# Kernel tuning notes

Measured on AMD Instinct MI355X. Metric: run time of the kernel, lower is better.

## Reference

```python
import jax, jax.numpy as jnp
import numpy as np

B, S, D = 4, 2048, 1024


def setup_inputs() -> dict:
    key = jax.random.key(0)
    kq, k1, k2, k3 = jax.random.split(key, 4)
    w_scale = 1.0 / np.sqrt(D)  # ~ glorot scale for square Dense
    q = jax.random.normal(kq, (B, S, D), dtype=jnp.float32)
    Wq = jax.random.normal(k1, (D, D), dtype=jnp.float32) * w_scale
    Wk = jax.random.normal(k2, (D, D), dtype=jnp.float32) * w_scale  # unused in self-attn path (bug in original)
    Wv = jax.random.normal(k3, (D, D), dtype=jnp.float32) * w_scale
    # causal mask: 1 = masked (future), matching tf.where(mask == 1, -1e9, scores)
    mask = jnp.triu(jnp.ones((S, S), dtype=jnp.int32), k=1)
    return {"q": q, "Wq": Wq, "Wk": Wk, "Wv": Wv, "mask": mask}


def reference(q, Wq, Wk, Wv, mask):
    # Self-attention path of the original: k=None, v=None.
    WQ = jnp.einsum('bsd,de->bse', q, Wq)
    # Faithful to the original code: dense_v is applied for BOTH K and V.
    WKV = jnp.einsum('bsd,de->bse', q, Wv)
    d_k = jnp.asarray(D, dtype=q.dtype)
    scores = jnp.einsum('bqd,bkd->bqk', WQ, WKV) / jnp.sqrt(d_k)  # [B,S,S]
    scores = jnp.where(mask == 1, jnp.asarray(-1e9, scores.dtype), scores)
    attn = jax.nn.softmax(scores, axis=-1)
    return jnp.einsum('bqk,bkd->bqd', attn, WKV)
```

## Files before the change

kernel.cpp:

```cpp
#include <hip/hip_runtime.h>


typedef unsigned short u16;
typedef short short8 __attribute__((ext_vector_type(8)));
typedef float floatx4 __attribute__((ext_vector_type(4)));

#define S_LEN 2048
#define D_DIM 1024
#define BK 64

__device__ inline u16 f2b(float f) {
  unsigned u = __float_as_uint(f);
  return (u16)((u + 0x7fffu + ((u >> 16) & 1u)) >> 16);
}

__device__ __forceinline__ void gload16(const u16* g, u16* l) {
  __builtin_amdgcn_global_load_lds(
      (const __attribute__((address_space(1))) void*)g,
      (__attribute__((address_space(3))) void*)l, 16, 0, 0);
}

__global__ __launch_bounds__(256)
void prep(const float* __restrict__ q, u16* __restrict__ qb16,
          const float* __restrict__ Wq, u16* __restrict__ Wqt,
          const float* __restrict__ Wv, u16* __restrict__ Wvt,
          float* __restrict__ rowsum) {
  int id = blockIdx.x, tid = threadIdx.x;
  if (id < 4096) {
    if (id < 4) {
      int o = id * 2048 + tid * 8;
      float4 zz = {0.f, 0.f, 0.f, 0.f};
      *(float4*)&rowsum[o] = zz;
      *(float4*)&rowsum[o + 4] = zz;
    }
    size_t idx = ((size_t)id * 256 + tid) * 8;
    float4 a0 = *(const float4*)&q[idx];
    float4 a1 = *(const float4*)&q[idx + 4];
    short8 v;
    v[0] = (short)f2b(a0.x); v[1] = (short)f2b(a0.y);
    v[2] = (short)f2b(a0.z); v[3] = (short)f2b(a0.w);
    v[4] = (short)f2b(a1.x); v[5] = (short)f2b(a1.y);
    v[6] = (short)f2b(a1.z); v[7] = (short)f2b(a1.w);
    *(short8*)&qb16[idx] = v;
    return;
  }
  __shared__ u16 tile[64][65];
  int id2 = id - 4096;
  int z = id2 >> 8;
  int idx4 = id2 & 255;
  int c0 = (idx4 & 15) * 64, r0 = (idx4 >> 4) * 64;
  const float* src = z ? Wv : Wq;
  u16* dst = z ? Wvt : Wqt;
  int tx = tid & 63, ty = tid >> 6;
#pragma unroll
  for (int i = 0; i < 16; ++i)
    tile[i * 4 + ty][tx] =
        f2b(src[(size_t)(r0 + i * 4 + ty) * 1024 + (c0 + tx)]);
  __syncthreads();
#pragma unroll
  for (int i = 0; i < 16; ++i)
    dst[(size_t)(c0 + i * 4 + ty) * 1024 + (r0 + tx)] = tile[tx][i * 4 + ty];
}

__global__ __launch_bounds__(512, 2)
void gemm_proj(const u16* __restrict__ A, const u16* __restrict__ B0,
               const u16* __restrict__ B1, u16* __restrict__ C0,
               u16* __restrict__ C1, u16* __restrict__ WKVt) {
  __shared__ __align__(16) u16 lds[65536];

  int id = blockIdx.x;
  int xcd = id & 7, i5 = id >> 3;
  int m_idx = xcd * 4 + (i5 & 3);
  int n_idx = i5 >> 2;
  int z = n_idx >> 2;
  int n0 = (n_idx & 3) * 256;
  int m0 = m_idx * 256;
  const u16* Bp = z ? B1 : B0;
  u16* Cp = z ? C1 : C0;

  int tid = threadIdx.x;
  int wv = tid >> 6, lane = tid & 63, quad = lane >> 4, l15 = lane & 15;
  int wm = wv >> 2, wn = wv & 3;

  int off_g[2];
#pragma unroll
  for (int l = 0; l < 2; ++l) {
    int chunk = (wv * 2 + l) * 64 + lane;
    int r = chunk >> 3, cs = chunk & 7;
    off_g[l] = r * 1024 + (cs ^ (r & 7)) * 8;
  }
  const u16* As0 = A + (size_t)m0 * 1024;
  const u16* As1 = A + (size_t)(m0 + 128) * 1024;
  const u16* Bs0 = Bp + (size_t)n0 * 1024;
  const u16* Bs1 = Bp + (size_t)(n0 + 128) * 1024;

#define PSTAGE(src, reg)                                                     \
  {                                                                          \
    _Pragma("unroll") for (int l = 0; l < 2; ++l)                            \
        gload16((src) + off_g[l], &lds[(reg) * 8192 + (wv * 2 + l) * 512]);  \
  }

  int aoff[2], boff[2];
#pragma unroll
  for (int kk = 0; kk < 2; ++kk) {
    int c = ((kk * 4 + quad) ^ (l15 & 7)) * 8;
    aoff[kk] = l15 * 64 + c;
    boff[kk] = ((wn & 1) * 64 + l15) * 64 + c;
  }
  const u16* A0p = &lds[(0 + wm) * 8192];
  const u16* A1p = &lds[(4 + wm) * 8192];
  const u16* B0p = &lds[(2 + (wn >> 1)) * 8192];
  const u16* B1p = &lds[(6 + (wn >> 1)) * 8192];

  floatx4 acc[8][4];
#pragma unroll
  for (int i = 0; i < 8; ++i)
#pragma unroll
    for (int j = 0; j < 4; ++j) acc[i][j] = (floatx4){0.f, 0.f, 0.f, 0.f};

#define BARp() __builtin_amdgcn_s_barrier()
#define WLG() asm volatile("s_waitcnt lgkmcnt(0)" ::: "memory")
#define WVM(n) asm volatile("s_waitcnt vmcnt(" #n ")" ::: "memory")

#define RDA(dst, base, fb)                                                 \
  _Pragma("unroll") for (int f = 0; f < 4; ++f)                            \
  _Pragma("unroll") for (int kk = 0; kk < 2; ++kk)                         \
      dst[f][kk] = *(const short8*)&(base)[((fb) + f) * 1024 + aoff[kk]];
#define RDB(dst, base, fb)                                                 \
  _Pragma("unroll") for (int f = 0; f < 2; ++f)                            \
  _Pragma("unroll") for (int kk = 0; kk < 2; ++kk)                         \
      dst[f][kk] = *(const short8*)&(base)[((fb) + f) * 1024 + boff[kk]];
#define MMQ(mh, nh, afq, bfq)                                              \
  __builtin_amdgcn_s_setprio(1);                                           \
  _Pragma("unroll") for (int f = 0; f < 4; ++f)                            \
  _Pragma("unroll") for (int g2 = 0; g2 < 2; ++g2)                         \
  _Pragma("unroll") for (int kk = 0; kk < 2; ++kk)                         \
      acc[(mh) * 4 + f][(nh) * 2 + g2] =                                   \
          __builtin_amdgcn_mfma_f32_16x16x32_bf16(                         \
              afq[f][kk], bfq[g2][kk], acc[(mh) * 4 + f][(nh) * 2 + g2],   \
              0, 0, 0);                                                    \
  __builtin_amdgcn_s_setprio(0);

  PSTAGE(As0, 0); PSTAGE(As1, 1); PSTAGE(Bs0, 2); PSTAGE(Bs1, 3);
  PSTAGE(As0 + 64, 4); PSTAGE(As1 + 64, 5); PSTAGE(Bs0 + 64, 6);
  PSTAGE(Bs1 + 64, 7);
  WVM(8);
  BARp();

#pragma unroll 1
  for (int it = 0; it < 8; ++it) {
    int kb2 = it * 128 + 128, kb3 = it * 128 + 192;
    short8 af[4][2], bf0[2][2], bf1[2][2];
    RDA(af, A0p, 0); RDB(bf0, B0p, 0);
    BARp(); WLG();
    MMQ(0, 0, af, bf0);
    BARp();
    RDB(bf1, B0p, 2);
    BARp(); WLG();
    MMQ(0, 1, af, bf1);
    BARp();
    RDA(af, A0p, 4);
    if (it < 7) PSTAGE(Bs0 + kb2, 2);
    BARp(); WLG();
    MMQ(1, 1, af, bf1);
    BARp();
    if (it < 7) { PSTAGE(Bs1 + kb2, 3); PSTAGE(As0 + kb2, 0); }
    BARp();
    MMQ(1, 0, af, bf0);
    if (it < 7) { WVM(6); } else { WVM(0); }
    BARp();
    RDA(af, A1p, 0); RDB(bf0, B1p, 0);
    if (it < 7) PSTAGE(As1 + kb2, 1);
    BARp(); WLG();
    MMQ(0, 0, af, bf0);
    BARp();
    RDB(bf1, B1p, 2);
    BARp(); WLG();
    MMQ(0, 1, af, bf1);
    BARp();
    RDA(af, A1p, 4);
    if (it < 7) PSTAGE(Bs0 + kb3, 6);
    BARp(); WLG();
    MMQ(1, 1, af, bf1);
    BARp();
    if (it < 7) {
      PSTAGE(Bs1 + kb3, 7); PSTAGE(As0 + kb3, 4); PSTAGE(As1 + kb3, 5);
    }
    BARp();
    MMQ(1, 0, af, bf0);
    if (it < 7) WVM(8);
    BARp();
  }

  asm volatile("s_waitcnt vmcnt(0) lgkmcnt(0)" ::: "memory");
#pragma unroll
  for (int mf = 0; mf < 8; ++mf)
#pragma unroll
    for (int nf = 0; nf < 4; ++nf)
#pragma unroll
      for (int r = 0; r < 4; ++r)
        Cp[(size_t)(m0 + wm * 128 + mf * 16 + quad * 4 + r) * D_DIM +
           (n0 + wn * 64 + nf * 16 + l15)] = f2b(acc[mf][nf][r]);

  if (z) {
    int b = m0 >> 11, srow = m0 & 2047;
    u16* Wt = WKVt + (size_t)b * D_DIM * S_LEN;
#pragma unroll
    for (int ph = 0; ph < 2; ++ph) {
      BARp();
      if ((wn >> 1) == ph) {
#pragma unroll
        for (int mf = 0; mf < 8; ++mf)
#pragma unroll
          for (int nf = 0; nf < 4; ++nf)
#pragma unroll
            for (int r = 0; r < 4; ++r)
              lds[((wn & 1) * 64 + nf * 16 + l15) * 272 +
                  (wm * 128 + mf * 16 + quad * 4 + r)] = f2b(acc[mf][nf][r]);
      }
      BARp();
#pragma unroll
      for (int rr = 0; rr < 8; ++rr) {
        int idx = rr * 512 + tid;
        int dl = idx >> 5, sc = idx & 31;
        *(short8*)&Wt[(size_t)(n0 + ph * 128 + dl) * S_LEN + srow + sc * 8] =
            *(const short8*)&lds[dl * 272 + sc * 8];
      }
    }
  }
}

#define GEMM64_PROLOG()                                                       \
  __shared__ __align__(16) u16 Als[2][64 * BK];                               \
  __shared__ __align__(16) u16 Bls[2][128 * BK];                              \
  int tid = threadIdx.x;                                                      \
  int wave = tid >> 6, lane = tid & 63, quad = lane >> 4, l15 = lane & 15;    \
  int wr = (wave >> 1) * 32, wc = (wave & 1) * 64;                            \
  int arow = lane >> 3;                                                       \
  int acol = ((lane & 7) ^ (arow & 7)) << 3;                                  \
  floatx4 acc[2][4];                                                          \
  _Pragma("unroll") for (int i = 0; i < 2; ++i)                               \
  _Pragma("unroll") for (int j = 0; j < 4; ++j)                               \
      acc[i][j] = (floatx4){0.f, 0.f, 0.f, 0.f};

#define GEMM64_STAGE(buf, Aptr, lda, Bptr, ldb, kb)                           \
  {                                                                           \
    _Pragma("unroll") for (int p = 0; p < 2; ++p) {                           \
      int r0 = wave * 16 + p * 8;                                             \
      gload16(&(Aptr)[(size_t)(m0 + r0 + arow) * (lda) + (kb) + acol],        \
              &Als[buf][r0 * BK]);                                            \
    }                                                                         \
    _Pragma("unroll") for (int p = 0; p < 4; ++p) {                           \
      int r0 = wave * 32 + p * 8;                                             \
      gload16(&(Bptr)[(size_t)(n0 + r0 + arow) * (ldb) + (kb) + acol],        \
              &Bls[buf][r0 * BK]);                                            \
    }                                                                         \
  }

#define GEMM64_KLOOP(Aptr, lda, Bptr, ldb, KEND)                              \
  GEMM64_STAGE(0, Aptr, lda, Bptr, ldb, 0);                                   \
  __syncthreads();                                                            \
  {                                                                           \
    int cur = 0;                                                              \
    for (int kb = 0; kb < (KEND); kb += BK, cur ^= 1) {                       \
      if (kb + BK < (KEND))                                                   \
        GEMM64_STAGE(cur ^ 1, Aptr, lda, Bptr, ldb, kb + BK);                 \
      const u16* Ab = &Als[cur][0];                                           \
      const u16* Bb = &Bls[cur][0];                                           \
      _Pragma("unroll") for (int kk8 = 0; kk8 < 8; kk8 += 4) {                \
        int cg = (((kk8 + quad) & 7) ^ (l15 & 7)) << 3;                       \
        short8 af[2], bfr[4];                                                 \
        _Pragma("unroll") for (int i = 0; i < 2; ++i)                         \
            af[i] = *(const short8*)&Ab[(wr + i * 16 + l15) * BK + cg];       \
        _Pragma("unroll") for (int j = 0; j < 4; ++j)                         \
            bfr[j] = *(const short8*)&Bb[(wc + j * 16 + l15) * BK + cg];      \
        _Pragma("unroll") for (int i = 0; i < 2; ++i)                         \
        _Pragma("unroll") for (int j = 0; j < 4; ++j)                         \
            acc[i][j] = __builtin_amdgcn_mfma_f32_16x16x32_bf16(              \
                af[i], bfr[j], acc[i][j], 0, 0, 0);                           \
      }                                                                       \
      __syncthreads();                                                        \
    }                                                                         \
  }

__global__ __launch_bounds__(256)
void gemm_scores(const u16* __restrict__ WQ, const u16* __restrict__ WKV,
                 u16* __restrict__ Pp, float* __restrict__ rowsum) {
  int id = blockIdx.x;
  int xcd = id & 7;
  int b = xcd & 3, h = xcd >> 2;
  int t = id >> 3;
  int m = (int)((sqrtf(8.f * (float)t + 1.f) - 1.f) * 0.5f);
  while ((m + 1) * (m + 2) / 2 <= t) ++m;
  while (m * (m + 1) / 2 > t) --m;
  int bj = t - m * (m + 1) / 2;
  int bi = 2 * m + h;
  int m0 = bi * 64, n0 = bj * 128;
  const u16* A = WQ + (size_t)b * S_LEN * D_DIM;
  const u16* Bp = WKV + (size_t)b * S_LEN * D_DIM;
  GEMM64_PROLOG();
  GEMM64_KLOOP(A, D_DIM, Bp, D_DIM, D_DIM);
  u16* Pb = Pp + (size_t)b * S_LEN * S_LEN;
  float part[2][4];
#pragma unroll
  for (int i = 0; i < 2; ++i)
#pragma unroll
    for (int r = 0; r < 4; ++r) part[i][r] = 0.f;
#pragma unroll
  for (int i = 0; i < 2; ++i)
#pragma unroll
    for (int j = 0; j < 4; ++j) {
      int col = n0 + wc + j * 16 + l15;
#pragma unroll
      for (int r = 0; r < 4; ++r) {
        int row = m0 + wr + i * 16 + quad * 4 + r;
        float p = (col > row) ? 0.f : __expf(acc[i][j][r] * 0.03125f);
        Pb[(size_t)row * S_LEN + col] = f2b(p);
        part[i][r] += p;
      }
    }
#pragma unroll
  for (int i = 0; i < 2; ++i)
#pragma unroll
    for (int r = 0; r < 4; ++r) {
      float v = part[i][r];
#pragma unroll
      for (int off = 1; off < 16; off <<= 1) v += __shfl_xor(v, off, 64);
      part[i][r] = v;
    }
  if (l15 == 0) {
#pragma unroll
    for (int i = 0; i < 2; ++i)
#pragma unroll
      for (int r = 0; r < 4; ++r)
        atomicAdd(&rowsum[b * S_LEN + m0 + wr + i * 16 + quad * 4 + r],
                  part[i][r]);
  }
}

__global__ __launch_bounds__(256)
void gemm_pv(const u16* __restrict__ Pp, const u16* __restrict__ WKVt,
             const float* __restrict__ rowsum, float* __restrict__ out) {
  int id = blockIdx.x;
  int xcd = id & 7;
  int b = xcd & 3, h = xcd >> 2;
  int r_ = id >> 3;
  int mh = 15 - (r_ >> 3);
  int bi = 2 * mh + h;
  int bj = r_ & 7;
  int m0 = bi * 64, n0 = bj * 128;
  int kend = (bi + 1) * 64;
  const u16* A = Pp + (size_t)b * S_LEN * S_LEN;
  const u16* Bp = WKVt + (size_t)b * (size_t)D_DIM * S_LEN;
  GEMM64_PROLOG();
  GEMM64_KLOOP(A, S_LEN, Bp, S_LEN, kend);
  const float* rs = rowsum + b * S_LEN;
  float* Co = out + (size_t)b * S_LEN * D_DIM;
#pragma unroll
  for (int i = 0; i < 2; ++i)
#pragma unroll
    for (int r = 0; r < 4; ++r) {
      int row = m0 + wr + i * 16 + quad * 4 + r;
      float inv = 1.0f / rs[row];
#pragma unroll
      for (int j = 0; j < 4; ++j)
        Co[(size_t)row * D_DIM + (n0 + wc + j * 16 + l15)] =
            acc[i][j][r] * inv;
    }
}

extern "C" void kernel_launch(void* const* d_in, const int* in_sizes, int n_in,
                              void* d_out, int out_size, void* d_ws, size_t ws_size,
                              hipStream_t stream) {
  const float* q = (const float*)d_in[0];
  const float* Wq = (const float*)d_in[1];
  const float* Wv = (const float*)d_in[3];
  char* ws = (char*)d_ws;
  const size_t MB = 1024 * 1024;
  u16* Wqt = (u16*)(ws);
  u16* Wvt = (u16*)(ws + 2 * MB);
  u16* qb16 = (u16*)(ws + 4 * MB);
  u16* Pp = (u16*)(ws);
  u16* WQ = (u16*)(ws + 32 * MB);
  u16* WKV = (u16*)(ws + 48 * MB);
  u16* WKVt = (u16*)(ws + 64 * MB);
  float* rowsum = (float*)(ws + 80 * MB);

  prep<<<4608, 256, 0, stream>>>(q, qb16, Wq, Wqt, Wv, Wvt, rowsum);
  gemm_proj<<<256, 512, 0, stream>>>(qb16, Wqt, Wvt, WQ, WKV, WKVt);
  gemm_scores<<<1088, 256, 0, stream>>>(WQ, WKV, Pp, rowsum);
  gemm_pv<<<1024, 256, 0, stream>>>(Pp, WKVt, rowsum, (float*)d_out);
}
```

Baseline: 212.9 us.

## Triple-buffer LDS stages in score and PV GEMMs with vmcnt-based waits

```diff
diff --git a/kernel.cpp b/kernel.cpp
--- a/kernel.cpp
+++ b/kernel.cpp
@@ -230,9 +230,9 @@
   }
 }
 
-#define GEMM64_PROLOG()                                                       \
-  __shared__ __align__(16) u16 Als[2][64 * BK];                               \
-  __shared__ __align__(16) u16 Bls[2][128 * BK];                              \
+#define GEMM64R_PROLOG()                                                      \
+  __shared__ __align__(16) u16 Als[3][64 * BK];                               \
+  __shared__ __align__(16) u16 Bls[3][128 * BK];                              \
   int tid = threadIdx.x;                                                      \
   int wave = tid >> 6, lane = tid & 63, quad = lane >> 4, l15 = lane & 15;    \
   int wr = (wave >> 1) * 32, wc = (wave & 1) * 64;                            \
@@ -243,7 +243,7 @@
   _Pragma("unroll") for (int j = 0; j < 4; ++j)                               \
       acc[i][j] = (floatx4){0.f, 0.f, 0.f, 0.f};
 
-#define GEMM64_STAGE(buf, Aptr, lda, Bptr, ldb, kb)                           \
+#define GEMM64R_STAGE(buf, Aptr, lda, Bptr, ldb, kb)                          \
   {                                                                           \
     _Pragma("unroll") for (int p = 0; p < 2; ++p) {                           \
       int r0 = wave * 16 + p * 8;                                             \
@@ -257,14 +257,21 @@
     }                                                                         \
   }
 
-#define GEMM64_KLOOP(Aptr, lda, Bptr, ldb, KEND)                              \
-  GEMM64_STAGE(0, Aptr, lda, Bptr, ldb, 0);                                   \
-  __syncthreads();                                                            \
+#define GEMM64R_KLOOP(Aptr, lda, Bptr, ldb, KEND)                             \
   {                                                                           \
-    int cur = 0;                                                              \
-    for (int kb = 0; kb < (KEND); kb += BK, cur ^= 1) {                       \
-      if (kb + BK < (KEND))                                                   \
-        GEMM64_STAGE(cur ^ 1, Aptr, lda, Bptr, ldb, kb + BK);                 \
+    const int NT = (KEND) / BK;                                               \
+    GEMM64R_STAGE(0, Aptr, lda, Bptr, ldb, 0);                                \
+    if (NT > 1) {                                                             \
+      GEMM64R_STAGE(1, Aptr, lda, Bptr, ldb, BK);                             \
+      WVM(6);                                                                 \
+    } else {                                                                  \
+      WVM(0);                                                                 \
+    }                                                                         \
+    BARp();                                                                   \
+    int cur = 0, stg = 2;                                                     \
+    _Pragma("unroll 1") for (int t = 0; t < NT; ++t) {                        \
+      if (t + 2 < NT)                                                         \
+        GEMM64R_STAGE(stg, Aptr, lda, Bptr, ldb, (t + 2) * BK);               \
       const u16* Ab = &Als[cur][0];                                           \
       const u16* Bb = &Bls[cur][0];                                           \
       _Pragma("unroll") for (int kk8 = 0; kk8 < 8; kk8 += 4) {                \
@@ -279,7 +286,10 @@
             acc[i][j] = __builtin_amdgcn_mfma_f32_16x16x32_bf16(              \
                 af[i], bfr[j], acc[i][j], 0, 0, 0);                           \
       }                                                                       \
-      __syncthreads();                                                        \
+      if (t + 2 < NT) { WVM(6); } else { WVM(0); }                            \
+      BARp();                                                                 \
+      if (++cur == 3) cur = 0;                                                \
+      if (++stg == 3) stg = 0;                                                \
     }                                                                         \
   }
 
@@ -298,8 +308,8 @@
   int m0 = bi * 64, n0 = bj * 128;
   const u16* A = WQ + (size_t)b * S_LEN * D_DIM;
   const u16* Bp = WKV + (size_t)b * S_LEN * D_DIM;
-  GEMM64_PROLOG();
-  GEMM64_KLOOP(A, D_DIM, Bp, D_DIM, D_DIM);
+  GEMM64R_PROLOG();
+  GEMM64R_KLOOP(A, D_DIM, Bp, D_DIM, D_DIM);
   u16* Pb = Pp + (size_t)b * S_LEN * S_LEN;
   float part[2][4];
 #pragma unroll
@@ -352,8 +362,8 @@
   int kend = (bi + 1) * 64;
   const u16* A = Pp + (size_t)b * S_LEN * S_LEN;
   const u16* Bp = WKVt + (size_t)b * (size_t)D_DIM * S_LEN;
-  GEMM64_PROLOG();
-  GEMM64_KLOOP(A, S_LEN, Bp, S_LEN, kend);
+  GEMM64R_PROLOG();
+  GEMM64R_KLOOP(A, S_LEN, Bp, S_LEN, kend);
   const float* rs = rowsum + b * S_LEN;
   float* Co = out + (size_t)b * S_LEN * D_DIM;
 #pragma unroll
```

Result: slower. 223.6 us (+5.0%).
